# Optimization experiments

Hardware: AMD Instinct MI355X
Metric: run time of the kernel (lower is better)

Reference implementation:

```python
import jax, jax.numpy as jnp
import numpy as np

N = 50000      # num_nodes
E = 300000     # edges per edge type
T = 3          # num_edge_type
C = 2          # num_channels
F_IN = 64      # feature_size
HID = 64       # hidden_size (w_out)
NL = 2         # num_layers (GT layers per FastGTN)
BETA = 0.5     # gtn_beta
TP = 0.8       # teleport_probability


def setup_inputs() -> dict:
    key = jax.random.key(0)
    ks = jax.random.split(key, 16)
    X = jax.random.normal(ks[0], (N, F_IN), dtype=jnp.float32)
    edge_index_0 = jax.random.randint(ks[1], (2, E), 0, N)
    edge_index_1 = jax.random.randint(ks[2], (2, E), 0, N)
    edge_index_2 = jax.random.randint(ks[3], (2, E), 0, N)
    edge_value_0 = jax.random.uniform(ks[4], (E,), dtype=jnp.float32)
    edge_value_1 = jax.random.uniform(ks[5], (E,), dtype=jnp.float32)
    edge_value_2 = jax.random.uniform(ks[6], (E,), dtype=jnp.float32)
    # glorot for Ws (per-channel projection), std=0.1 for GT layer mixing weights
    g0 = np.sqrt(6.0 / (F_IN + HID))
    g1 = np.sqrt(6.0 / (HID + HID))
    Ws0 = jax.random.uniform(ks[7], (C, F_IN, HID), minval=-g0, maxval=g0, dtype=jnp.float32)
    Ws1 = jax.random.uniform(ks[8], (C, HID, HID), minval=-g1, maxval=g1, dtype=jnp.float32)
    layerW0 = 0.1 * jax.random.normal(ks[9], (NL, C, T), dtype=jnp.float32)
    layerW1 = 0.1 * jax.random.normal(ks[10], (NL, C, T), dtype=jnp.float32)
    gl = np.sqrt(1.0 / (C * HID))
    lin_W0 = jax.random.uniform(ks[11], (C * HID, HID), minval=-gl, maxval=gl, dtype=jnp.float32)
    lin_b0 = jax.random.uniform(ks[12], (HID,), minval=-gl, maxval=gl, dtype=jnp.float32)
    lin_W1 = jax.random.uniform(ks[13], (C * HID, HID), minval=-gl, maxval=gl, dtype=jnp.float32)
    lin_b1 = jax.random.uniform(ks[14], (HID,), minval=-gl, maxval=gl, dtype=jnp.float32)
    return dict(X=X,
                edge_value_0=edge_value_0, edge_value_1=edge_value_1, edge_value_2=edge_value_2,
                Ws0=Ws0, Ws1=Ws1, layerW0=layerW0, layerW1=layerW1,
                lin_W0=lin_W0, lin_b0=lin_b0, lin_W1=lin_W1, lin_b1=lin_b1,
                edge_index_0=edge_index_0, edge_index_1=edge_index_1, edge_index_2=edge_index_2)


def _spmm_mix(H, filt, vals, etype, row, col):
    # H: [C, N, d]; filt: [C, T] softmaxed; vals: [Etot]; etype/row/col: [Etot]
    # == for each channel c: sum_j filt[c,j] * (A_j @ H[c])
    w = vals[None, :] * filt[:, etype]          # [C, Etot]
    msg = w[:, :, None] * H[:, col, :]          # [C, Etot, d]
    return jax.vmap(lambda m: jax.ops.segment_sum(m, row, num_segments=N))(msg)


def _fastgtn_block(Xin, Ws, layerW, linW, linb, row, col, vals, etype):
    H = jnp.einsum('nf,cfo->cno', Xin, Ws)      # [C, N, HID]
    X0 = jax.lax.stop_gradient(H)               # X_ = H.clone().detach()
    for l in range(NL):
        filt = jax.nn.softmax(layerW[l], axis=1)
        H = _spmm_mix(H, filt, vals, etype, row, col)
    Hm = TP * jax.nn.relu(BETA * X0 + (1.0 - BETA) * H) + (1.0 - TP) * X0
    Hm = jnp.transpose(Hm, (1, 0, 2)).reshape(N, C * Hm.shape[-1])  # [N, C*HID]
    return jax.nn.relu(Hm @ linW + linb)


def reference(X, edge_value_0, edge_value_1, edge_value_2,
              Ws0, Ws1, layerW0, layerW1,
              lin_W0, lin_b0, lin_W1, lin_b1,
              edge_index_0, edge_index_1, edge_index_2):
    row = jnp.concatenate([edge_index_0[0], edge_index_1[0], edge_index_2[0]])
    col = jnp.concatenate([edge_index_0[1], edge_index_1[1], edge_index_2[1]])
    vals = jnp.concatenate([edge_value_0, edge_value_1, edge_value_2])
    etype = jnp.repeat(jnp.arange(T), E)
    H = _fastgtn_block(X, Ws0, layerW0, lin_W0, lin_b0, row, col, vals, etype)
    H = _fastgtn_block(H, Ws1, layerW1, lin_W1, lin_b1, row, col, vals, etype)
    return H
```

## Files before the change

### kernel.cpp

```cpp
#include <hip/hip_runtime.h>
#include <hip/hip_fp16.h>

#define NN 50000
#define EE 300000
#define ETOT (3 * EE)
#define HD 64
#define RB 256
#define NB 196
#define CHUNK 8192
#define NBLKT ((EE + CHUNK - 1) / CHUNK)
#define NBT (3 * NBLKT)
#define NTOT (NB * NBT)
#define GS_VPT ((NTOT + 1023) / 1024)
#define MAXB 6144


__global__ void filt_kernel(const float* __restrict__ lw0,
                            const float* __restrict__ lw1,
                            float* __restrict__ filt) {
    int i = threadIdx.x;
    if (i < 8) {
        int b = i >> 2, l = (i >> 1) & 1, c = i & 1;
        const float* lw = (b == 0 ? lw0 : lw1) + l * 6 + c * 3;
        float a0 = lw[0], a1 = lw[1], a2 = lw[2];
        float m  = fmaxf(a0, fmaxf(a1, a2));
        float e0 = expf(a0 - m), e1 = expf(a1 - m), e2 = expf(a2 - m);
        float s  = e0 + e1 + e2;
        float* o = filt + i * 3;
        o[0] = e0 / s; o[1] = e1 / s; o[2] = e2 / s;
    }
}

__global__ void __launch_bounds__(256)
hist1_kernel(const int* __restrict__ ei0, const int* __restrict__ ei1,
             const int* __restrict__ ei2, int* __restrict__ hist) {
    __shared__ int lh[NB];
    int t = blockIdx.y;
    const int* ei = (t == 0) ? ei0 : (t == 1) ? ei1 : ei2;
    int tid = threadIdx.x;
    for (int i = tid; i < NB; i += 256) lh[i] = 0;
    __syncthreads();
    int e0 = blockIdx.x * CHUNK;
    for (int it = 0; it < CHUNK / 256; ++it) {
        int e = e0 + it * 256 + tid;
        if (e < EE) atomicAdd(&lh[ei[e] >> 8], 1);
    }
    __syncthreads();
    int flat = t * NBLKT + blockIdx.x;
    for (int i = tid; i < NB; i += 256) hist[flat * NB + i] = lh[i];
}

__global__ void __launch_bounds__(1024)
gscan_kernel(const int* __restrict__ hist, int* __restrict__ gbase,
             int* __restrict__ bbase, int* __restrict__ rp) {
    __shared__ int wsum[16];
    int tid = threadIdx.x, lane = tid & 63, wv = tid >> 6;
    int s0 = tid * GS_VPT;
    int local = 0;
    for (int j = 0; j < GS_VPT; ++j) {
        int s = s0 + j;
        if (s < NTOT) {
            int bucket = s / NBT, flat = s - bucket * NBT;
            local += hist[flat * NB + bucket];
        }
    }
    int x = local;
#pragma unroll
    for (int d = 1; d < 64; d <<= 1) {
        int y = __shfl_up(x, d);
        if (lane >= d) x += y;
    }
    if (lane == 63) wsum[wv] = x;
    __syncthreads();
    if (tid == 0) {
        int s = 0;
        for (int i = 0; i < 16; ++i) { int t = wsum[i]; wsum[i] = s; s += t; }
    }
    __syncthreads();
    int run = x + wsum[wv] - local;
    for (int j = 0; j < GS_VPT; ++j) {
        int s = s0 + j;
        if (s < NTOT) {
            int bucket = s / NBT, flat = s - bucket * NBT;
            gbase[flat * NB + bucket] = run;
            if (flat == 0) bbase[bucket] = run;
            run += hist[flat * NB + bucket];
        }
    }
    if (tid == 0) { bbase[NB] = ETOT; rp[NN] = ETOT; }
}

__global__ void __launch_bounds__(256)
place_kernel(const int* __restrict__ ei0, const int* __restrict__ ei1,
             const int* __restrict__ ei2,
             const float* __restrict__ ev0, const float* __restrict__ ev1,
             const float* __restrict__ ev2,
             const int* __restrict__ gbase, uint2* __restrict__ staged) {
    __shared__ int lbase[NB];
    int t = blockIdx.y;
    const int*   ei = (t == 0) ? ei0 : (t == 1) ? ei1 : ei2;
    const float* ev = (t == 0) ? ev0 : (t == 1) ? ev1 : ev2;
    int tid = threadIdx.x;
    int flat = t * NBLKT + blockIdx.x;
    for (int i = tid; i < NB; i += 256) lbase[i] = gbase[flat * NB + i];
    __syncthreads();
    int e0 = blockIdx.x * CHUNK;
    for (int it = 0; it < CHUNK / 256; ++it) {
        int e = e0 + it * 256 + tid;
        if (e < EE) {
            int row = ei[e];
            int col = ei[EE + e];
            unsigned int q = (unsigned int)__float2int_rn(ev[e] * 16383.0f);
            unsigned int mw = (unsigned int)col | ((unsigned int)t << 16) | (q << 18);
            int pos = atomicAdd(&lbase[row >> 8], 1);
            staged[pos] = make_uint2(mw, (unsigned int)row);
        }
    }
}

__global__ void __launch_bounds__(256)
csr_kernel(const uint2* __restrict__ staged, const int* __restrict__ bbase,
           int* __restrict__ rp, unsigned int* __restrict__ meta) {
    __shared__ int hist[RB];
    __shared__ int lcur[RB];
    __shared__ int wsum[4];
    __shared__ unsigned int metaL[MAXB];
    int b   = blockIdx.x;
    int tid = threadIdx.x;
    int base = bbase[b];
    int cnt  = bbase[b + 1] - base;
    int row0 = b * RB;

    hist[tid] = 0;
    __syncthreads();
    for (int i = tid; i < cnt; i += 256) {
        uint2 s = staged[base + i];
        atomicAdd(&hist[(int)s.y - row0], 1);
    }
    __syncthreads();
    int lane = tid & 63, wv = tid >> 6;
    int v = hist[tid];
    int x = v;
#pragma unroll
    for (int d = 1; d < 64; d <<= 1) {
        int y = __shfl_up(x, d);
        if (lane >= d) x += y;
    }
    if (lane == 63) wsum[wv] = x;
    __syncthreads();
    if (tid == 0) {
        int s = 0;
        for (int i = 0; i < 4; ++i) { int t = wsum[i]; wsum[i] = s; s += t; }
    }
    __syncthreads();
    int excl = x + wsum[wv] - v;
    lcur[tid] = excl;
    int row = row0 + tid;
    if (row < NN) rp[row] = base + excl;
    __syncthreads();
    for (int i = tid; i < cnt; i += 256) {
        uint2 s = staged[base + i];
        int p = atomicAdd(&lcur[(int)s.y - row0], 1);
        metaL[p] = s.x;
    }
    __syncthreads();
    for (int i = tid; i < cnt; i += 256)
        meta[base + i] = metaL[i];
}

#define PROJ_NTILE (NN / 16)
__global__ void __launch_bounds__(256)
proj_kernel(const float* __restrict__ Xin, const float* __restrict__ Ws,
            __half2* __restrict__ Hh) {
    __shared__ float Wl[2 * 64 * 64];
    __shared__ float Xs[16 * 65];
    int tid = threadIdx.x;
    for (int i = tid; i < 2 * 64 * 64; i += 256) Wl[i] = Ws[i];
    int oq = (tid & 15) * 4;
    int ln = tid >> 4;
    for (int tile = blockIdx.x; tile < PROJ_NTILE; tile += gridDim.x) {
        int n0 = tile * 16;
        __syncthreads();
        for (int i = tid; i < 16 * 64; i += 256)
            Xs[(i >> 6) * 65 + (i & 63)] = Xin[(n0 + (i >> 6)) * 64 + (i & 63)];
        __syncthreads();
        float a0[4] = {0.f, 0.f, 0.f, 0.f};
        float a1[4] = {0.f, 0.f, 0.f, 0.f};
        for (int f = 0; f < 64; ++f) {
            float  x  = Xs[ln * 65 + f];
            float4 w0 = *(const float4*)&Wl[f * 64 + oq];
            float4 w1 = *(const float4*)&Wl[4096 + f * 64 + oq];
            a0[0] += x * w0.x; a0[1] += x * w0.y;
            a0[2] += x * w0.z; a0[3] += x * w0.w;
            a1[0] += x * w1.x; a1[1] += x * w1.y;
            a1[2] += x * w1.z; a1[3] += x * w1.w;
        }
        float4 o4;
        ((__half2*)&o4)[0] = __floats2half2_rn(a0[0], a1[0]);
        ((__half2*)&o4)[1] = __floats2half2_rn(a0[1], a1[1]);
        ((__half2*)&o4)[2] = __floats2half2_rn(a0[2], a1[2]);
        ((__half2*)&o4)[3] = __floats2half2_rn(a0[3], a1[3]);
        *(float4*)&Hh[(n0 + ln) * HD + oq] = o4;
    }
}

__global__ void __launch_bounds__(256)
spmm_kernel(const float4* __restrict__ Hin4, float4* __restrict__ Hout4,
            const unsigned int* __restrict__ meta, const int* __restrict__ rp,
            const float* __restrict__ filt ) {
    const int wid  = threadIdx.x >> 6;
    const int lane = threadIdx.x & 63;
    const int g    = lane >> 4;
    const int fq   = lane & 15;
    const int row  = blockIdx.x * 4 + wid;

    const float s = 1.0f / 16383.0f;
    const float F00 = filt[0] * s, F01 = filt[1] * s, F02 = filt[2] * s;
    const float F10 = filt[3] * s, F11 = filt[4] * s, F12 = filt[5] * s;

    float accA[4] = {0.f, 0.f, 0.f, 0.f};
    float accB[4] = {0.f, 0.f, 0.f, 0.f};

    const int beg = rp[row], end = rp[row + 1];
    for (int j0 = beg; j0 < end; j0 += 64) {
        int cnt = min(end - j0, 64);
        unsigned int m = (lane < cnt) ? meta[j0 + lane] : 0u;
        for (int k = 0; k < cnt; k += 8) {
            unsigned int mmA = (unsigned int)__shfl((int)m, k + g);
            unsigned int mmB = (unsigned int)__shfl((int)m, k + 4 + g);
            float4 rA = Hin4[(mmA & 0xffffu) * 16 + fq];
            float4 rB = Hin4[(mmB & 0xffffu) * 16 + fq];
            int   etA = (mmA >> 16) & 3,  etB = (mmB >> 16) & 3;
            float qA  = (float)(mmA >> 18), qB = (float)(mmB >> 18);
            float w0A = qA * ((etA == 0) ? F00 : (etA == 1) ? F01 : F02);
            float w1A = qA * ((etA == 0) ? F10 : (etA == 1) ? F11 : F12);
            float w0B = qB * ((etB == 0) ? F00 : (etB == 1) ? F01 : F02);
            float w1B = qB * ((etB == 0) ? F10 : (etB == 1) ? F11 : F12);
#pragma unroll
            for (int i = 0; i < 4; ++i) {
                float2 xA = __half22float2(((const __half2*)&rA)[i]);
                float2 xB = __half22float2(((const __half2*)&rB)[i]);
                accA[i] += w0A * xA.x + w0B * xB.x;
                accB[i] += w1A * xA.y + w1B * xB.y;
            }
        }
    }
#pragma unroll
    for (int i = 0; i < 4; ++i) {
        accA[i] += __shfl_xor(accA[i], 16); accA[i] += __shfl_xor(accA[i], 32);
        accB[i] += __shfl_xor(accB[i], 16); accB[i] += __shfl_xor(accB[i], 32);
    }
    if (g == 0) {
        float4 o4;
        ((__half2*)&o4)[0] = __floats2half2_rn(accA[0], accB[0]);
        ((__half2*)&o4)[1] = __floats2half2_rn(accA[1], accB[1]);
        ((__half2*)&o4)[2] = __floats2half2_rn(accA[2], accB[2]);
        ((__half2*)&o4)[3] = __floats2half2_rn(accA[3], accB[3]);
        Hout4[row * 16 + fq] = o4;
    }
}

#define EPI_TILE 64
#define HS_STRIDE 132
__global__ void __launch_bounds__(256)
epilogue_kernel(const __half2* __restrict__ X0, const __half2* __restrict__ H,
                const float* __restrict__ linW, const float* __restrict__ linb,
                float* __restrict__ out) {
    __shared__ float Wl[128 * 64];
    __shared__ float Hs[EPI_TILE * HS_STRIDE];
    int tid = threadIdx.x;
    for (int i = tid; i < 128 * 64; i += 256) Wl[i] = linW[i];
    int oq = tid & 15, nq = tid >> 4;
    float bias[4];
#pragma unroll
    for (int i = 0; i < 4; ++i) bias[i] = linb[oq + 16 * i];
    const int ntiles = (NN + EPI_TILE - 1) / EPI_TILE;
    for (int tile = blockIdx.x; tile < ntiles; tile += gridDim.x) {
        int n0 = tile * EPI_TILE;
        __syncthreads();
        for (int i = tid; i < EPI_TILE * 64; i += 256) {
            int ln = i >> 6, d = i & 63;
            int n = n0 + ln;
            float2 x0 = make_float2(0.f, 0.f), h = make_float2(0.f, 0.f);
            if (n < NN) {
                x0 = __half22float2(X0[n * HD + d]);
                h  = __half22float2(H [n * HD + d]);
            }
            float z0 = fmaxf(0.5f * x0.x + 0.5f * h.x, 0.f);
            float z1 = fmaxf(0.5f * x0.y + 0.5f * h.y, 0.f);
            Hs[ln * HS_STRIDE + d]      = 0.8f * z0 + 0.2f * x0.x;
            Hs[ln * HS_STRIDE + 64 + d] = 0.8f * z1 + 0.2f * x0.y;
        }
        __syncthreads();
        float acc[4][4];
#pragma unroll
        for (int j = 0; j < 4; ++j)
#pragma unroll
            for (int i = 0; i < 4; ++i) acc[j][i] = bias[i];
        for (int k = 0; k < 128; k += 4) {
            float4 hq[4];
#pragma unroll
            for (int j = 0; j < 4; ++j)
                hq[j] = *(const float4*)&Hs[(nq + 16 * j) * HS_STRIDE + k];
#pragma unroll
            for (int kk = 0; kk < 4; ++kk) {
                float w[4];
#pragma unroll
                for (int i = 0; i < 4; ++i) w[i] = Wl[(k + kk) * 64 + oq + 16 * i];
#pragma unroll
                for (int j = 0; j < 4; ++j) {
                    float x = (kk == 0) ? hq[j].x : (kk == 1) ? hq[j].y
                             : (kk == 2) ? hq[j].z : hq[j].w;
#pragma unroll
                    for (int i = 0; i < 4; ++i) acc[j][i] += x * w[i];
                }
            }
        }
#pragma unroll
        for (int j = 0; j < 4; ++j) {
            int n = n0 + nq + 16 * j;
            if (n < NN) {
#pragma unroll
                for (int i = 0; i < 4; ++i)
                    out[n * HD + oq + 16 * i] = fmaxf(acc[j][i], 0.f);
            }
        }
    }
}

extern "C" void kernel_launch(void* const* d_in, const int* in_sizes, int n_in,
                              void* d_out, int out_size, void* d_ws, size_t ws_size,
                              hipStream_t stream) {
    const float* X     = (const float*)d_in[0];
    const float* ev0   = (const float*)d_in[1];
    const float* ev1   = (const float*)d_in[2];
    const float* ev2   = (const float*)d_in[3];
    const float* Ws0   = (const float*)d_in[4];
    const float* Ws1   = (const float*)d_in[5];
    const float* lw0   = (const float*)d_in[6];
    const float* lw1   = (const float*)d_in[7];
    const float* linW0 = (const float*)d_in[8];
    const float* linb0 = (const float*)d_in[9];
    const float* linW1 = (const float*)d_in[10];
    const float* linb1 = (const float*)d_in[11];
    const int*   ei0   = (const int*)d_in[12];
    const int*   ei1   = (const int*)d_in[13];
    const int*   ei2   = (const int*)d_in[14];
    float* out = (float*)d_out;

    float* ws = (float*)d_ws;
    __half2* X0h = (__half2*)(ws);
    __half2* Ha  = (__half2*)(ws + 1 * NN * HD);
    __half2* Hb  = (__half2*)(ws + 2 * NN * HD);
    float*   mid = ws + 3 * NN * HD;
    uint2*   staged = (uint2*)mid;
    float*   filt   = ws + 4 * NN * HD;
    int*     hist   = (int*)(filt + 32);
    int*     gbase  = hist + NTOT;
    int*     bbase  = gbase + NTOT;
    int*     rp     = bbase + NB + 4;
    unsigned int* meta = (unsigned int*)(rp + NN + 16);

    filt_kernel<<<1, 64, 0, stream>>>(lw0, lw1, filt);
    dim3 egrid(NBLKT, 3);
    hist1_kernel<<<egrid, 256, 0, stream>>>(ei0, ei1, ei2, hist);
    gscan_kernel<<<1, 1024, 0, stream>>>(hist, gbase, bbase, rp);
    place_kernel<<<egrid, 256, 0, stream>>>(ei0, ei1, ei2, ev0, ev1, ev2,
                                            gbase, staged);
    csr_kernel<<<NB, 256, 0, stream>>>(staged, bbase, rp, meta);

    proj_kernel<<<512, 256, 0, stream>>>(X, Ws0, X0h);
    spmm_kernel<<<NN / 4, 256, 0, stream>>>((const float4*)X0h, (float4*)Ha,
                                            meta, rp, filt + 0);
    spmm_kernel<<<NN / 4, 256, 0, stream>>>((const float4*)Ha, (float4*)Hb,
                                            meta, rp, filt + 6);
    epilogue_kernel<<<512, 256, 0, stream>>>(X0h, Hb, linW0, linb0, mid);

    proj_kernel<<<512, 256, 0, stream>>>(mid, Ws1, X0h);
    spmm_kernel<<<NN / 4, 256, 0, stream>>>((const float4*)X0h, (float4*)Ha,
                                            meta, rp, filt + 12);
    spmm_kernel<<<NN / 4, 256, 0, stream>>>((const float4*)Ha, (float4*)Hb,
                                            meta, rp, filt + 18);
    epilogue_kernel<<<512, 256, 0, stream>>>(X0h, Hb, linW1, linb1, out);
}
```

Baseline: 414.5 us.

## Fold filter softmax into scan and co-schedule edge placement with first projection

```diff
diff --git a/kernel.cpp b/kernel.cpp
--- a/kernel.cpp
+++ b/kernel.cpp
@@ -13,23 +13,9 @@
 #define NTOT (NB * NBT)
 #define GS_VPT ((NTOT + 1023) / 1024)
 #define MAXB 6144
-
-
-__global__ void filt_kernel(const float* __restrict__ lw0,
-                            const float* __restrict__ lw1,
-                            float* __restrict__ filt) {
-    int i = threadIdx.x;
-    if (i < 8) {
-        int b = i >> 2, l = (i >> 1) & 1, c = i & 1;
-        const float* lw = (b == 0 ? lw0 : lw1) + l * 6 + c * 3;
-        float a0 = lw[0], a1 = lw[1], a2 = lw[2];
-        float m  = fmaxf(a0, fmaxf(a1, a2));
-        float e0 = expf(a0 - m), e1 = expf(a1 - m), e2 = expf(a2 - m);
-        float s  = e0 + e1 + e2;
-        float* o = filt + i * 3;
-        o[0] = e0 / s; o[1] = e1 / s; o[2] = e2 / s;
-    }
-}
+#define PROJ_NTILE (NN / 16)
+#define PP_GRID (NBT + 512)
+
 
 __global__ void __launch_bounds__(256)
 hist1_kernel(const int* __restrict__ ei0, const int* __restrict__ ei1,
@@ -52,9 +38,21 @@
 
 __global__ void __launch_bounds__(1024)
 gscan_kernel(const int* __restrict__ hist, int* __restrict__ gbase,
-             int* __restrict__ bbase, int* __restrict__ rp) {
+             int* __restrict__ bbase, int* __restrict__ rp,
+             const float* __restrict__ lw0, const float* __restrict__ lw1,
+             float* __restrict__ filt) {
     __shared__ int wsum[16];
     int tid = threadIdx.x, lane = tid & 63, wv = tid >> 6;
+    if (tid < 8) {
+        int b = tid >> 2, l = (tid >> 1) & 1, c = tid & 1;
+        const float* lw = (b == 0 ? lw0 : lw1) + l * 6 + c * 3;
+        float a0 = lw[0], a1 = lw[1], a2 = lw[2];
+        float m  = fmaxf(a0, fmaxf(a1, a2));
+        float e0 = expf(a0 - m), e1 = expf(a1 - m), e2 = expf(a2 - m);
+        float s  = e0 + e1 + e2;
+        float* o = filt + tid * 3;
+        o[0] = e0 / s; o[1] = e1 / s; o[2] = e2 / s;
+    }
     int s0 = tid * GS_VPT;
     int local = 0;
     for (int j = 0; j < GS_VPT; ++j) {
@@ -91,29 +89,65 @@
 }
 
 __global__ void __launch_bounds__(256)
-place_kernel(const int* __restrict__ ei0, const int* __restrict__ ei1,
-             const int* __restrict__ ei2,
-             const float* __restrict__ ev0, const float* __restrict__ ev1,
-             const float* __restrict__ ev2,
-             const int* __restrict__ gbase, uint2* __restrict__ staged) {
-    __shared__ int lbase[NB];
-    int t = blockIdx.y;
-    const int*   ei = (t == 0) ? ei0 : (t == 1) ? ei1 : ei2;
-    const float* ev = (t == 0) ? ev0 : (t == 1) ? ev1 : ev2;
+place_proj_kernel(const int* __restrict__ ei0, const int* __restrict__ ei1,
+                  const int* __restrict__ ei2,
+                  const float* __restrict__ ev0, const float* __restrict__ ev1,
+                  const float* __restrict__ ev2,
+                  const int* __restrict__ gbase, uint2* __restrict__ staged,
+                  const float* __restrict__ Xin, const float* __restrict__ Ws,
+                  __half2* __restrict__ Hh) {
+    __shared__ float Wl[2 * 64 * 64];
+    __shared__ float Xs[16 * 65];
+    __shared__ int   lbase[NB];
     int tid = threadIdx.x;
-    int flat = t * NBLKT + blockIdx.x;
-    for (int i = tid; i < NB; i += 256) lbase[i] = gbase[flat * NB + i];
-    __syncthreads();
-    int e0 = blockIdx.x * CHUNK;
-    for (int it = 0; it < CHUNK / 256; ++it) {
-        int e = e0 + it * 256 + tid;
-        if (e < EE) {
-            int row = ei[e];
-            int col = ei[EE + e];
-            unsigned int q = (unsigned int)__float2int_rn(ev[e] * 16383.0f);
-            unsigned int mw = (unsigned int)col | ((unsigned int)t << 16) | (q << 18);
-            int pos = atomicAdd(&lbase[row >> 8], 1);
-            staged[pos] = make_uint2(mw, (unsigned int)row);
+
+    if (blockIdx.x < NBT) {
+        int flat = blockIdx.x;
+        int t  = flat / NBLKT;
+        int bx = flat - t * NBLKT;
+        const int*   ei = (t == 0) ? ei0 : (t == 1) ? ei1 : ei2;
+        const float* ev = (t == 0) ? ev0 : (t == 1) ? ev1 : ev2;
+        for (int i = tid; i < NB; i += 256) lbase[i] = gbase[flat * NB + i];
+        __syncthreads();
+        int e0 = bx * CHUNK;
+        for (int it = 0; it < CHUNK / 256; ++it) {
+            int e = e0 + it * 256 + tid;
+            if (e < EE) {
+                int row = ei[e];
+                int col = ei[EE + e];
+                unsigned int q = (unsigned int)__float2int_rn(ev[e] * 16383.0f);
+                unsigned int mw = (unsigned int)col | ((unsigned int)t << 16) | (q << 18);
+                int pos = atomicAdd(&lbase[row >> 8], 1);
+                staged[pos] = make_uint2(mw, (unsigned int)row);
+            }
+        }
+    } else {
+        for (int i = tid; i < 2 * 64 * 64; i += 256) Wl[i] = Ws[i];
+        int oq = (tid & 15) * 4;
+        int ln = tid >> 4;
+        for (int tile = blockIdx.x - NBT; tile < PROJ_NTILE; tile += 512) {
+            int n0 = tile * 16;
+            __syncthreads();
+            for (int i = tid; i < 16 * 64; i += 256)
+                Xs[(i >> 6) * 65 + (i & 63)] = Xin[(n0 + (i >> 6)) * 64 + (i & 63)];
+            __syncthreads();
+            float a0[4] = {0.f, 0.f, 0.f, 0.f};
+            float a1[4] = {0.f, 0.f, 0.f, 0.f};
+            for (int f = 0; f < 64; ++f) {
+                float  x  = Xs[ln * 65 + f];
+                float4 w0 = *(const float4*)&Wl[f * 64 + oq];
+                float4 w1 = *(const float4*)&Wl[4096 + f * 64 + oq];
+                a0[0] += x * w0.x; a0[1] += x * w0.y;
+                a0[2] += x * w0.z; a0[3] += x * w0.w;
+                a1[0] += x * w1.x; a1[1] += x * w1.y;
+                a1[2] += x * w1.z; a1[3] += x * w1.w;
+            }
+            float4 o4;
+            ((__half2*)&o4)[0] = __floats2half2_rn(a0[0], a1[0]);
+            ((__half2*)&o4)[1] = __floats2half2_rn(a0[1], a1[1]);
+            ((__half2*)&o4)[2] = __floats2half2_rn(a0[2], a1[2]);
+            ((__half2*)&o4)[3] = __floats2half2_rn(a0[3], a1[3]);
+            *(float4*)&Hh[(n0 + ln) * HD + oq] = o4;
         }
     }
 }
@@ -168,7 +202,6 @@
         meta[base + i] = metaL[i];
 }
 
-#define PROJ_NTILE (NN / 16)
 __global__ void __launch_bounds__(256)
 proj_kernel(const float* __restrict__ Xin, const float* __restrict__ Ws,
             __half2* __restrict__ Hh) {
@@ -361,15 +394,16 @@
     int*     rp     = bbase + NB + 4;
     unsigned int* meta = (unsigned int*)(rp + NN + 16);
 
-    filt_kernel<<<1, 64, 0, stream>>>(lw0, lw1, filt);
     dim3 egrid(NBLKT, 3);
     hist1_kernel<<<egrid, 256, 0, stream>>>(ei0, ei1, ei2, hist);
-    gscan_kernel<<<1, 1024, 0, stream>>>(hist, gbase, bbase, rp);
-    place_kernel<<<egrid, 256, 0, stream>>>(ei0, ei1, ei2, ev0, ev1, ev2,
-                                            gbase, staged);
+    gscan_kernel<<<1, 1024, 0, stream>>>(hist, gbase, bbase, rp,
+                                         lw0, lw1, filt);
+    place_proj_kernel<<<PP_GRID, 256, 0, stream>>>(ei0, ei1, ei2,
+                                                   ev0, ev1, ev2,
+                                                   gbase, staged,
+                                                   X, Ws0, X0h);
     csr_kernel<<<NB, 256, 0, stream>>>(staged, bbase, rp, meta);
 
-    proj_kernel<<<512, 256, 0, stream>>>(X, Ws0, X0h);
     spmm_kernel<<<NN / 4, 256, 0, stream>>>((const float4*)X0h, (float4*)Ha,
                                             meta, rp, filt + 0);
     spmm_kernel<<<NN / 4, 256, 0, stream>>>((const float4*)Ha, (float4*)Hb,
```

Result: faster. 392.8 us (-5.3%).
